# Kernel tuning notes

Measured on AMD Instinct MI355X. Metric: run time of the kernel, lower is better.

## Reference

```python
import jax, jax.numpy as jnp
from jax import lax
import numpy as np

LEVELS = 17
VAR_N = 4
UNITS = 3 * LEVELS          # 51 neurons: motor 17, command 13, inter 21
MOTOR = LEVELS
PRED_N = 4
UNFOLDS = 6                 # ncps LTC default ode_unfolds
EPS = 1e-8
B = 32768                   # recurrence length = B + PRED_N
D = VAR_N * LEVELS          # 68


def _build_wiring(seed=0):
    # AutoNCP(51, 17, sparsity_level=0.8): inter=21, command=13, motor=17
    # sensory_fanout=4, inter_fanout=2, 5 recurrent command synapses, motor_fanin=2
    rng = np.random.default_rng(seed)
    motor, command, S = 17, 13, LEVELS
    N = UNITS
    cmd = np.arange(motor, motor + command)
    intr = np.arange(motor + command, N)
    adj = np.zeros((N, N), np.float32)
    sadj = np.zeros((S, N), np.float32)
    pol = lambda: float(rng.choice([-1.0, 1.0]))
    for s in range(S):
        for d in rng.choice(intr, 4, replace=False):
            sadj[s, d] = pol()
    for d in intr:
        if not sadj[:, d].any():
            sadj[int(rng.integers(S)), d] = pol()
    for i in intr:
        for d in rng.choice(cmd, 2, replace=False):
            adj[i, d] = pol()
    for d in cmd:
        if not adj[intr, d].any():
            adj[int(rng.choice(intr)), d] = pol()
    for _ in range(5):
        adj[int(rng.choice(cmd)), int(rng.choice(cmd))] = pol()
    for m in range(motor):
        for srci in rng.choice(cmd, 2, replace=False):
            adj[srci, m] = pol()
    return adj, sadj


def setup_inputs():
    key = jax.random.key(0)
    ks = iter(jax.random.split(key, 48))
    u = lambda s, lo, hi: jax.random.uniform(next(ks), s, jnp.float32, lo, hi)
    lin = lambda i, o: jax.random.normal(next(ks), (i, o), jnp.float32) * (i ** -0.5)
    adj, sadj = _build_wiring()
    V, N, S = VAR_N, UNITS, LEVELS
    M1 = (LEVELS + D) // 2           # 42
    G = VAR_N * D                    # 272
    G2 = (G + D) // 2                # 170
    return dict(
        x=jax.random.normal(next(ks), (B, D), jnp.float32),
        pre_w1=lin(D, D), pre_b1=jnp.zeros((D,), jnp.float32),
        pre_w2=lin(D, D), pre_b2=jnp.zeros((D,), jnp.float32),
        gleak=u((V, N), 0.001, 1.0), vleak=u((V, N), -0.2, 0.2), cm=u((V, N), 0.4, 0.6),
        w=u((V, N, N), 0.001, 1.0), sigma=u((V, N, N), 3.0, 8.0), mu=u((V, N, N), 0.3, 0.8),
        erev=jnp.asarray(np.tile(adj, (V, 1, 1))),
        sens_w=u((V, S, N), 0.001, 1.0), sens_sigma=u((V, S, N), 3.0, 8.0), sens_mu=u((V, S, N), 0.3, 0.8),
        sens_erev=jnp.asarray(np.tile(sadj, (V, 1, 1))),
        in_w=jnp.ones((V, S), jnp.float32), in_b=jnp.zeros((V, S), jnp.float32),
        out_w=jnp.ones((V, MOTOR), jnp.float32), out_b=jnp.zeros((V, MOTOR), jnp.float32),
        tW1=lin(LEVELS, LEVELS), tb1=jnp.zeros((LEVELS,), jnp.float32),
        tW2=lin(LEVELS, M1), tb2=jnp.zeros((M1,), jnp.float32),
        tW3=lin(M1, D), tb3=jnp.zeros((D,), jnp.float32),
        gW1=lin(G, G), gb1=jnp.zeros((G,), jnp.float32),
        gW2=lin(G, G2), gb2=jnp.zeros((G2,), jnp.float32),
        gW3=lin(G2, D), gb3=jnp.zeros((D,), jnp.float32),
        mask=jnp.asarray((adj != 0).astype(np.float32)),
        sens_mask=jnp.asarray((sadj != 0).astype(np.float32)),
    )


def _forward(x, pre_w1, pre_b1, pre_w2, pre_b2,
             gleak, vleak, cm, w, sigma, mu, erev,
             sens_w, sens_sigma, sens_mu, sens_erev,
             in_w, in_b, out_w, out_b,
             tW1, tb1, tW2, tb2, tW3, tb3,
             gW1, gb1, gW2, gb2, gW3, gb3,
             mask, sens_mask, ckpt=False):
    sig = jax.nn.sigmoid
    # VarEncoder: Linear -> Sigmoid -> Linear
    h = sig(x @ pre_w1 + pre_b1) @ pre_w2 + pre_b2                  # (B, 68)
    xs = h.reshape(-1, VAR_N, LEVELS).transpose(1, 0, 2)            # (V, B, 17)
    seqs = jnp.concatenate([xs, jnp.repeat(xs[:, -1:, :], PRED_N, axis=1)], axis=1)  # (V, T, 17)

    def run(p, seq):
        gl_, vl_, cm_, w_, sg_, mu_, er_, sw_, ssg_, smu_, ser_, iw_, ib_, ow_, ob_ = p
        gl = jax.nn.softplus(gl_)                 # (N,)
        wp = jax.nn.softplus(w_) * mask           # (N, N) sparse NCP wiring
        swp = jax.nn.softplus(sw_) * sens_mask    # (S, N)
        cmt = jax.nn.softplus(cm_) * UNFOLDS      # cm / (elapsed=1 / unfolds)

        def step(v, u_in):
            u = u_in * iw_ + ib_                                   # affine input mapping
            sact = swp * sig((u[:, None] - smu_) * ssg_)           # (S, N)
            num_s = (sact * ser_).sum(0)
            den_s = sact.sum(0)

            def unfold(vv, _):
                wa = wp * sig((vv[:, None] - mu_) * sg_)           # (N, N), src axis 0
                vv = (cmt * vv + gl * vl_ + (wa * er_).sum(0) + num_s) / (
                    cmt + gl + wa.sum(0) + den_s + EPS)
                return vv, None

            v, _ = lax.scan(unfold, v, None, length=UNFOLDS)
            return v, v[:MOTOR] * ow_ + ob_                        # affine output mapping

        stepf = jax.checkpoint(step) if ckpt else step
        _, outs = lax.scan(stepf, jnp.zeros((UNITS,), seq.dtype), seq)
        return outs                                                # (T, 17)

    p = (gleak, vleak, cm, w, sigma, mu, erev,
         sens_w, sens_sigma, sens_mu, sens_erev, in_w, in_b, out_w, out_b)
    rs = jax.vmap(run, in_axes=(0, 0))(p, seqs)                    # (V, T, 17)
    r = rs.transpose(1, 0, 2)                                      # (T, V, 17)
    # CrossConnector: per-tile MLP 17->17->42->68 (sigmoids), flatten, 272->272->170->68
    t = sig(sig(sig(r @ tW1 + tb1) @ tW2 + tb2) @ tW3 + tb3)        # (T, V, 68)
    g = t.reshape(t.shape[0], -1)                                   # (T, 272)
    return sig(sig(g @ gW1 + gb1) @ gW2 + gb2) @ gW3 + gb3          # (T, 68)


def reference(x, pre_w1, pre_b1, pre_w2, pre_b2,
              gleak, vleak, cm, w, sigma, mu, erev,
              sens_w, sens_sigma, sens_mu, sens_erev,
              in_w, in_b, out_w, out_b,
              tW1, tb1, tW2, tb2, tW3, tb3,
              gW1, gb1, gW2, gb2, gW3, gb3,
              mask, sens_mask):
    return _forward(x, pre_w1, pre_b1, pre_w2, pre_b2,
                    gleak, vleak, cm, w, sigma, mu, erev,
                    sens_w, sens_sigma, sens_mu, sens_erev,
                    in_w, in_b, out_w, out_b,
                    tW1, tb1, tW2, tb2, tW3, tb3,
                    gW1, gb1, gW2, gb2, gW3, gb3,
                    mask, sens_mask)
```

## Files before the change

### kernel.cpp

```cpp
#include <hip/hip_runtime.h>
#include <hip/hip_bf16.h>
#include <math.h>

#define LEVELS 17
#define VARN   4
#define UNITS  51
#define MOTOR  17
#define NB     32768
#define TT     (NB + 4)
#define DD     68
#define LOG2E  1.4426950408889634f
#define TROWS  16

#define W_WARM  10
#define L_CHUNK 34
#define NCHUNK  ((TT + L_CHUNK - 1) / L_CHUNK)

#define W_F     64
#define L_F     64
#define NCHUNK_F ((TT + L_F - 1) / L_F)
#define CAP_R  16

#define MROWS  48
#define MBLK   ((TT + MROWS - 1) / MROWS)
#define EBLK   ((NB + MROWS - 1) / MROWS)
#define BUFSZ  (48 * 272 + 64)
#define EBUFSZ (48 * 72 + 64)

#define OFF_WA 0
#define OFF_WB 7680
#define OFF_WC 24576
#define OFF_WD 76800
#define OFF_WE 155136
#define OFF_WF 205824
#define OFF_P1 221184
#define OFF_P2 228864
#define WTS_SHORTS 236544
#define PSENS_N (VARN * LEVELS * UNITS)

typedef __attribute__((ext_vector_type(8))) short short8v;
typedef __attribute__((ext_vector_type(4))) float f32x4;

__device__ __forceinline__ float fast_rcp(float x) { return __builtin_amdgcn_rcpf(x); }
__device__ __forceinline__ float fast_exp2(float x) { return __builtin_amdgcn_exp2f(x); }
__device__ __forceinline__ float sigf(float x) { return fast_rcp(1.0f + __expf(-x)); }
__device__ __forceinline__ float softplusf(float x) { return logf(1.0f + expf(x)); }
__device__ __forceinline__ unsigned short f2bf(float x) {
    unsigned int u = __float_as_uint(x);
    unsigned int r = u + 0x7FFFu + ((u >> 16) & 1u);
    return (unsigned short)(r >> 16);
}

__global__ __launch_bounds__(256) void prep_weights(
    const float* __restrict__ tW1, const float* __restrict__ tW2, const float* __restrict__ tW3,
    const float* __restrict__ gW1, const float* __restrict__ gW2, const float* __restrict__ gW3,
    const float* __restrict__ pW1, const float* __restrict__ pW2,
    unsigned short* __restrict__ wts)
{
    const int ph = blockIdx.y;
    const int KTt[8]   = {3, 3, 6, 9, 9, 6, 3, 3};
    const int NCt[8]   = {5, 11, 17, 17, 11, 5, 5, 5};
    const int offsT[8] = {OFF_WA, OFF_WB, OFF_WC, OFF_WD, OFF_WE, OFF_WF, OFF_P1, OFF_P2};
    int S = NCt[ph] * KTt[ph] * 512;
    int idx = blockIdx.x * 256 + threadIdx.x;
    if (idx >= S) return;
    int tile = idx >> 9;
    int r    = idx & 511;
    int lane = r >> 3;
    int e    = r & 7;
    int KTp  = KTt[ph];
    int ct   = tile / KTp;
    int kt   = tile - ct * KTp;
    int n = ct * 16 + (lane & 15);
    int k = kt * 32 + (lane >> 4) * 8 + e;
    float val = 0.0f;
    switch (ph) {
        case 0: if (k < 68 && n < 68) { int v = k / 17; if (n / 17 == v) val = tW1[(k % 17) * 17 + (n % 17)]; } break;
        case 1: if (k < 68 && n < 168) { int v = k / 17; int c = n - 42 * v; if (c >= 0 && c < 42) val = tW2[(k % 17) * 42 + c]; } break;
        case 2: if (k < 168 && n < 272) { int v = k / 42; int c = n - 68 * v; if (c >= 0 && c < 68) val = tW3[(k % 42) * 68 + c]; } break;
        case 3: if (k < 272 && n < 272) val = gW1[k * 272 + n]; break;
        case 4: if (k < 272 && n < 170) val = gW2[k * 170 + n]; break;
        case 5: if (k < 170 && n < 68)  val = gW3[k * 68 + n]; break;
        case 6: if (k < 68 && n < 68)   val = pW1[k * 68 + n]; break;
        case 7: if (k < 68 && n < 68)   val = pW2[k * 68 + n]; break;
    }
    wts[offsT[ph] + idx] = f2bf(val);
}

__global__ __launch_bounds__(256) void prep_sens(
    const float* __restrict__ sens_w, const float* __restrict__ sens_sigma,
    const float* __restrict__ sens_mu, const float* __restrict__ sens_erev,
    float4* __restrict__ psens)
{
    int idx = blockIdx.x * 256 + threadIdx.x;
    if (idx >= PSENS_N) return;
    float sg = sens_sigma[idx], m = sens_mu[idx];
    float wf = softplusf(sens_w[idx]);
    psens[idx] = make_float4(fast_exp2(sg * m * LOG2E), -sg * LOG2E, wf, wf * sens_erev[idx]);
}

template<int KT, int NC>
__device__ __forceinline__ void mfma_phase(
    const unsigned short* __restrict__ wt,
    const unsigned short* __restrict__ bufIn, int ldkIn,
    unsigned short* __restrict__ bufOut, int ldkOut,
    const float* __restrict__ bias, int bmod, int Nvalid,
    int lane, int wave)
{
    #pragma unroll
    for (int rt = 0; rt < 3; ++rt) {
        short8v af[KT];
        int abase = (rt * 16 + (lane & 15)) * ldkIn + 8 * (lane >> 4);
        #pragma unroll
        for (int kt = 0; kt < KT; ++kt)
            af[kt] = *reinterpret_cast<const short8v*>(&bufIn[abase + kt * 32]);
        for (int ct = wave; ct < NC; ct += 4) {
            int c = ct * 16 + (lane & 15);
            const unsigned short* wp = wt + (size_t)(ct * KT) * 512 + lane * 8;
            short8v bf[KT];
            #pragma unroll
            for (int kt = 0; kt < KT; ++kt)
                bf[kt] = *reinterpret_cast<const short8v*>(&wp[kt * 512]);
            f32x4 acc = {0.0f, 0.0f, 0.0f, 0.0f};
            #pragma unroll
            for (int kt = 0; kt < KT; ++kt)
                acc = __builtin_amdgcn_mfma_f32_16x16x32_bf16(af[kt], bf[kt], acc, 0, 0, 0);
            float bv = 0.0f;
            if (c < Nvalid) {
                int cb = (bmod == 0) ? (c % 17) : (bmod == 1) ? (c % 42) : (bmod == 2) ? (c % 68) : c;
                bv = bias[cb];
            }
            #pragma unroll
            for (int i = 0; i < 4; ++i) {
                float vv = sigf(acc[i] + bv);
                int rl = rt * 16 + (lane >> 4) * 4 + i;
                if (c < ldkOut) bufOut[rl * ldkOut + c] = f2bf(vv);
            }
        }
    }
}

template<int KT>
__device__ __forceinline__ void mfma_final(
    const unsigned short* __restrict__ wt,
    const unsigned short* __restrict__ bufIn, int ldkIn,
    float* __restrict__ io, int baseRow,
    const float* __restrict__ gb3, int lane, int wave)
{
    #pragma unroll
    for (int rt = 0; rt < 3; ++rt) {
        short8v af[KT];
        int abase = (rt * 16 + (lane & 15)) * ldkIn + 8 * (lane >> 4);
        #pragma unroll
        for (int kt = 0; kt < KT; ++kt)
            af[kt] = *reinterpret_cast<const short8v*>(&bufIn[abase + kt * 32]);
        for (int ct = wave; ct < 5; ct += 4) {
            int c = ct * 16 + (lane & 15);
            const unsigned short* wp = wt + (size_t)(ct * KT) * 512 + lane * 8;
            short8v bf[KT];
            #pragma unroll
            for (int kt = 0; kt < KT; ++kt)
                bf[kt] = *reinterpret_cast<const short8v*>(&wp[kt * 512]);
            f32x4 acc = {0.0f, 0.0f, 0.0f, 0.0f};
            #pragma unroll
            for (int kt = 0; kt < KT; ++kt)
                acc = __builtin_amdgcn_mfma_f32_16x16x32_bf16(af[kt], bf[kt], acc, 0, 0, 0);
            float bv = (c < 68) ? gb3[c] : 0.0f;
            #pragma unroll
            for (int i = 0; i < 4; ++i) {
                int row = baseRow + rt * 16 + (lane >> 4) * 4 + i;
                if (c < 68 && row < TT) io[(size_t)row * DD + c] = acc[i] + bv;
            }
        }
    }
}

__global__ __launch_bounds__(256) void mlp_mfma(
    float* __restrict__ io, const unsigned short* __restrict__ wts,
    const float* __restrict__ tb1, const float* __restrict__ tb2, const float* __restrict__ tb3,
    const float* __restrict__ gb1, const float* __restrict__ gb2, const float* __restrict__ gb3)
{
    __shared__ unsigned short buf0[BUFSZ];
    __shared__ unsigned short buf1[BUFSZ];
    int tid = threadIdx.x, lane = tid & 63, wave = tid >> 6;
    int baseRow = blockIdx.x * MROWS;

    for (int e = tid; e < BUFSZ; e += 256) { buf0[e] = 0; buf1[e] = 0; }
    __syncthreads();
    for (int e = tid; e < MROWS * DD; e += 256) {
        int r = e / DD, c = e % DD;
        int gr = baseRow + r;
        float xv = (gr < TT) ? io[(size_t)gr * DD + c] : 0.0f;
        buf0[r * 72 + c] = f2bf(xv);
    }
    __syncthreads();
    mfma_phase<3, 5 >(wts + OFF_WA, buf0, 72,  buf1, 72,  tb1, 0, 68,  lane, wave); __syncthreads();
    mfma_phase<3, 11>(wts + OFF_WB, buf1, 72,  buf0, 168, tb2, 1, 168, lane, wave); __syncthreads();
    mfma_phase<6, 17>(wts + OFF_WC, buf0, 168, buf1, 272, tb3, 2, 272, lane, wave); __syncthreads();
    mfma_phase<9, 17>(wts + OFF_WD, buf1, 272, buf0, 272, gb1, 3, 272, lane, wave); __syncthreads();
    mfma_phase<9, 11>(wts + OFF_WE, buf0, 272, buf1, 176, gb2, 3, 170, lane, wave); __syncthreads();
    mfma_final<6>(wts + OFF_WF, buf1, 176, io, baseRow, gb3, lane, wave);
}

__global__ __launch_bounds__(256) void enc_mfma(
    const float* __restrict__ x, const unsigned short* __restrict__ wts,
    const float* __restrict__ pb1, const float* __restrict__ pb2,
    float* __restrict__ seq)
{
    __shared__ unsigned short buf0[EBUFSZ];
    __shared__ unsigned short buf1[EBUFSZ];
    int tid = threadIdx.x, lane = tid & 63, wave = tid >> 6;
    int baseRow = blockIdx.x * MROWS;

    for (int e = tid; e < EBUFSZ; e += 256) { buf0[e] = 0; buf1[e] = 0; }
    __syncthreads();
    for (int e = tid; e < MROWS * DD; e += 256) {
        int r = e / DD, c = e % DD;
        int gr = baseRow + r;
        float xv = (gr < NB) ? x[(size_t)gr * DD + c] : 0.0f;
        buf0[r * 72 + c] = f2bf(xv);
    }
    __syncthreads();
    mfma_phase<3, 5>(wts + OFF_P1, buf0, 72, buf1, 72, pb1, 3, 68, lane, wave);
    __syncthreads();
    #pragma unroll
    for (int rt = 0; rt < 3; ++rt) {
        short8v af[3];
        int abase = (rt * 16 + (lane & 15)) * 72 + 8 * (lane >> 4);
        #pragma unroll
        for (int kt = 0; kt < 3; ++kt)
            af[kt] = *reinterpret_cast<const short8v*>(&buf1[abase + kt * 32]);
        for (int ct = wave; ct < 5; ct += 4) {
            int c = ct * 16 + (lane & 15);
            const unsigned short* wp = wts + OFF_P2 + (size_t)(ct * 3) * 512 + lane * 8;
            short8v bf[3];
            #pragma unroll
            for (int kt = 0; kt < 3; ++kt)
                bf[kt] = *reinterpret_cast<const short8v*>(&wp[kt * 512]);
            f32x4 acc = {0.0f, 0.0f, 0.0f, 0.0f};
            #pragma unroll
            for (int kt = 0; kt < 3; ++kt)
                acc = __builtin_amdgcn_mfma_f32_16x16x32_bf16(af[kt], bf[kt], acc, 0, 0, 0);
            float bv = (c < 68) ? pb2[c] : 0.0f;
            #pragma unroll
            for (int i = 0; i < 4; ++i) {
                int row = baseRow + rt * 16 + (lane >> 4) * 4 + i;
                if (c < 68 && row < NB) {
                    float vv = acc[i] + bv;
                    int v = c / 17, s = c % 17;
                    float* dst = seq + ((size_t)v * TT + row) * LEVELS + s;
                    dst[0] = vv;
                    if (row == NB - 1) {
                        dst[1 * LEVELS] = vv; dst[2 * LEVELS] = vv;
                        dst[3 * LEVELS] = vv; dst[4 * LEVELS] = vv;
                    }
                }
            }
        }
    }
}

#define SENS_TPW 16
__global__ __launch_bounds__(256) void sens_kernel(
    const float* __restrict__ seq,
    const float4* __restrict__ psens,
    const float* __restrict__ in_w, const float* __restrict__ in_b,
    const float* __restrict__ sens_mask,
    float2* __restrict__ tab)
{
    int gwi = blockIdx.x * 4 + (threadIdx.x >> 6);
    int j   = threadIdx.x & 63;
    int v    = gwi & 3;
    int tbase = (gwi >> 2) * SENS_TPW;
    if (tbase >= TT) return;

    unsigned int bits0 = 0;
    if (j < UNITS)
        for (int s = 0; s < LEVELS; ++s)
            bits0 |= (sens_mask[s * UNITS + j] != 0.0f ? 1u : 0u) << s;
    int ns = __popc(bits0);
    int mS = ns;
    #pragma unroll
    for (int off = 32; off; off >>= 1) mS = max(mS, __shfl_xor(mS, off, 64));

    float iw = (j < LEVELS) ? in_w[v * LEVELS + j] : 0.0f;
    float ib = (j < LEVELS) ? in_b[v * LEVELS + j] : 0.0f;

    int tend = min(TT, tbase + SENS_TPW);
    for (int t = tbase; t < tend; ++t) {
        float u = (j < LEVELS)
            ? fmaf(seq[((size_t)v * TT + t) * LEVELS + j], iw, ib) : 0.0f;
        unsigned int bits = bits0;
        float num = 0.0f, den = 0.0f;
        for (int k = 0; k < mS; ++k) {
            bool on = (k < ns) && (bits != 0u);
            int s = on ? (__ffs(bits) - 1) : 0;
            if (on) bits &= bits - 1;
            float us = __shfl(u, s, 64);
            float4 p = psens[(v * LEVELS + s) * UNITS + (j < UNITS ? j : 0)];
            float g = fast_rcp(fmaf(p.x, fast_exp2(p.y * us), 1.0f));
            if (on) { num = fmaf(p.w, g, num); den = fmaf(p.z, g, den); }
        }
        if (j < UNITS)
            tab[((size_t)v * TT + t) * UNITS + j] = make_float2(num, den);
    }
}

template<int MH>
__device__ void scan_body(
    int j, int jn, bool hasHelp, int partner, int myStart, int myCnt,
    unsigned long long colbits, int v, int t0, int wstart, int tend,
    float cmt, float glvl, float cgl, float ow, float ob, bool isHelper,
    const float* __restrict__ w, const float* __restrict__ sigma,
    const float* __restrict__ mu, const float* __restrict__ erev,
    const float2* __restrict__ tab, float* __restrict__ rout)
{
    int   src[MH]; float fw[MH], fc[MH], fk[MH], fwfe[MH];
    unsigned long long bits = colbits;
    for (int s = 0; s < myStart; ++s) bits &= bits - 1;
    #pragma unroll
    for (int k = 0; k < MH; ++k) {
        bool on = (k < myCnt);
        int sc = on ? (__ffsll((unsigned long long)bits) - 1) : 0;
        src[k] = sc;
        size_t pi = ((size_t)v * UNITS + sc) * UNITS + jn;
        float sg = on ? sigma[pi] : 0.0f;
        float m  = on ? mu[pi]    : 0.0f;
        fw[k] = on ? softplusf(w[pi]) : 0.0f;
        fc[k] = fast_exp2(sg * m * LOG2E);
        fk[k] = -sg * LOG2E;
        fwfe[k] = on ? fw[k] * erev[pi] : 0.0f;
        if (on) bits &= bits - 1;
    }
    const float2* tp = tab + (size_t)v * TT * UNITS + jn;
    float* rp = rout + (size_t)v * LEVELS + j;
    float2 nd = tp[(size_t)t0 * UNITS];
    float vreg = 0.0f;
    for (int t = t0; t < tend; ++t) {
        float2 ndc = nd;
        if (t + 1 < tend) nd = tp[(size_t)(t + 1) * UNITS];
        float bn = isHelper ? 0.0f : (glvl + ndc.x);
        float bd = isHelper ? 0.0f : (cgl + ndc.y);
        #pragma unroll
        for (int uf = 0; uf < 6; ++uf) {
            float vs[MH];
            #pragma unroll
            for (int k = 0; k < MH; ++k) vs[k] = __shfl(vreg, src[k], 64);
            float num = bn, den = bd;
            #pragma unroll
            for (int k = 0; k < MH; ++k) {
                float g = fast_rcp(fmaf(fc[k], fast_exp2(fk[k] * vs[k]), 1.0f));
                num = fmaf(fwfe[k], g, num);
                den = fmaf(fw[k], g, den);
            }
            float pn = __shfl(num, partner, 64);
            float pd = __shfl(den, partner, 64);
            if (hasHelp) { num += pn; den += pd; }
            vreg = fmaf(cmt, vreg, num) * fast_rcp(den);
        }
        if (j < MOTOR && t >= wstart) rp[(size_t)t * DD] = fmaf(vreg, ow, ob);
    }
}

__device__ void scan_body_gen(
    int j, int jn, bool hasHelp, int partner, int myStart, int myCnt, int mcMax,
    unsigned long long colbits, int v, int t0, int wstart, int tend,
    float cmt, float glvl, float cgl, float ow, float ob, bool isHelper,
    const float* __restrict__ w, const float* __restrict__ sigma,
    const float* __restrict__ mu, const float* __restrict__ erev,
    const float2* __restrict__ tab, float* __restrict__ rout)
{
    unsigned long long mybits = colbits;
    for (int s = 0; s < myStart; ++s) mybits &= mybits - 1;
    const float2* tp = tab + (size_t)v * TT * UNITS + jn;
    float* rp = rout + (size_t)v * LEVELS + j;
    float vreg = 0.0f;
    for (int t = t0; t < tend; ++t) {
        float2 ndc = tp[(size_t)t * UNITS];
        float bn = isHelper ? 0.0f : (glvl + ndc.x);
        float bd = isHelper ? 0.0f : (cgl + ndc.y);
        for (int uf = 0; uf < 6; ++uf) {
            unsigned long long bits = mybits;
            float num = bn, den = bd;
            for (int k = 0; k < mcMax; ++k) {
                bool on = (k < myCnt) && (bits != 0ull);
                int sc = on ? (__ffsll(bits) - 1) : 0;
                if (on) bits &= bits - 1;
                float vs = __shfl(vreg, sc, 64);
                size_t pi = ((size_t)v * UNITS + sc) * UNITS + jn;
                float a = on ? softplusf(w[pi]) * sigf((vs - mu[pi]) * sigma[pi]) : 0.0f;
                num = fmaf(a, on ? erev[pi] : 0.0f, num);
                den += a;
            }
            float pn = __shfl(num, partner, 64);
            float pd = __shfl(den, partner, 64);
            if (hasHelp) { num += pn; den += pd; }
            vreg = fmaf(cmt, vreg, num) * fast_rcp(den);
        }
        if (j < MOTOR && t >= wstart) rp[(size_t)t * DD] = fmaf(vreg, ow, ob);
    }
}

__global__ __launch_bounds__(256, 8) void scan_pre(
    const float2* __restrict__ tab,
    const float* __restrict__ gleak, const float* __restrict__ vleak, const float* __restrict__ cm,
    const float* __restrict__ w, const float* __restrict__ sigma,
    const float* __restrict__ mu, const float* __restrict__ erev,
    const float* __restrict__ out_w, const float* __restrict__ out_b,
    const float* __restrict__ mask,
    float* __restrict__ rout)
{
    int gwi = (blockIdx.x << 2) + (threadIdx.x >> 6);
    int j = threadIdx.x & 63;
    int v = gwi & 3;
    int chunk = gwi >> 2;
    if (chunk >= NCHUNK) return;
    int wstart = chunk * L_CHUNK;
    int tend = min(TT, wstart + L_CHUNK);
    int t0 = max(0, wstart - W_WARM);

    bool isHelper = (j >= UNITS);
    int jn = isHelper ? (j - 34) : j;
    unsigned long long colbits = 0ull;
    for (int i = 0; i < UNITS; ++i)
        colbits |= (unsigned long long)(mask[i * UNITS + jn] != 0.0f ? 1 : 0) << i;
    int nf = __popcll(colbits);
    bool isCmd = (jn >= MOTOR && jn < MOTOR + 13);
    int nh = (nf + 1) >> 1;
    int myStart, myCnt;
    if (isHelper)    { myStart = nh; myCnt = nf - nh; }
    else if (isCmd)  { myStart = 0;  myCnt = nh; }
    else             { myStart = 0;  myCnt = nf; }
    bool hasHelp = (!isHelper) && isCmd;
    int partner = hasHelp ? (jn + 34) : j;

    float cmt  = softplusf(cm[v * UNITS + jn]) * 6.0f;
    float gl   = softplusf(gleak[v * UNITS + jn]);
    float glvl = gl * vleak[v * UNITS + jn];
    float cgl  = cmt + gl + 1e-8f;
    float ow = (j < MOTOR) ? out_w[v * LEVELS + j] : 0.0f;
    float ob = (j < MOTOR) ? out_b[v * LEVELS + j] : 0.0f;

    int mc = myCnt;
    #pragma unroll
    for (int off = 32; off; off >>= 1) mc = max(mc, __shfl_xor(mc, off, 64));

    if (mc <= 4)
        scan_body<4>(j, jn, hasHelp, partner, myStart, myCnt, colbits, v, t0, wstart, tend,
                     cmt, glvl, cgl, ow, ob, isHelper, w, sigma, mu, erev, tab, rout);
    else if (mc <= 6)
        scan_body<6>(j, jn, hasHelp, partner, myStart, myCnt, colbits, v, t0, wstart, tend,
                     cmt, glvl, cgl, ow, ob, isHelper, w, sigma, mu, erev, tab, rout);
    else if (mc <= 8)
        scan_body<8>(j, jn, hasHelp, partner, myStart, myCnt, colbits, v, t0, wstart, tend,
                     cmt, glvl, cgl, ow, ob, isHelper, w, sigma, mu, erev, tab, rout);
    else
        scan_body_gen(j, jn, hasHelp, partner, myStart, myCnt, mc, colbits, v, t0, wstart, tend,
                      cmt, glvl, cgl, ow, ob, isHelper, w, sigma, mu, erev, tab, rout);
}

__global__ __launch_bounds__(128) void enc_kernel(
    const float* __restrict__ x,
    const float* __restrict__ W1, const float* __restrict__ b1,
    const float* __restrict__ W2, const float* __restrict__ b2,
    float* __restrict__ seq)
{
    int t = blockIdx.x;
    int j = threadIdx.x;
    __shared__ float xs[DD];
    __shared__ float h1[DD];
    if (j < DD) xs[j] = x[(size_t)t * DD + j];
    __syncthreads();
    if (j < DD) {
        float acc = b1[j];
        #pragma unroll 4
        for (int k = 0; k < DD; ++k) acc = fmaf(xs[k], W1[k * DD + j], acc);
        h1[j] = sigf(acc);
    }
    __syncthreads();
    if (j < DD) {
        float acc = b2[j];
        #pragma unroll 4
        for (int k = 0; k < DD; ++k) acc = fmaf(h1[k], W2[k * DD + j], acc);
        int v = j / LEVELS, s = j % LEVELS;
        float* dst = seq + ((size_t)v * TT + t) * LEVELS + s;
        dst[0] = acc;
        if (t == NB - 1) {
            dst[1 * LEVELS] = acc; dst[2 * LEVELS] = acc;
            dst[3 * LEVELS] = acc; dst[4 * LEVELS] = acc;
        }
    }
}

template<int MF, int MS>
__device__ __forceinline__ void scan_loop_f(
    int j, int v, int t0, int wstart, int tend,
    const float* __restrict__ seq, float* __restrict__ rout,
    float cmt, float glvl, float cgl, float iw, float ib, float ow, float ob,
    int nf, int ns,
    const int* rs_, const float* rw_, const float* rc_, const float* rk_, const float* re_,
    const int* ss_, const float* sw_, const float* sc_, const float* sk_, const float* se_)
{
    int fs[MF]; float fw[MF], fc[MF], fk[MF], fe[MF];
    #pragma unroll
    for (int k = 0; k < MF; ++k) {
        bool on = k < nf;
        int idx = j * CAP_R + k;
        fs[k] = on ? rs_[idx] : 0;
        fw[k] = on ? rw_[idx] : 0.0f;
        fc[k] = on ? rc_[idx] : 1.0f;
        fk[k] = on ? rk_[idx] : 0.0f;
        fe[k] = on ? re_[idx] : 0.0f;
    }
    int gs[MS]; float gw[MS], gc[MS], gk[MS], ge[MS];
    #pragma unroll
    for (int k = 0; k < MS; ++k) {
        bool on = k < ns;
        int idx = j * LEVELS + k;
        gs[k] = on ? ss_[idx] : 0;
        gw[k] = on ? sw_[idx] : 0.0f;
        gc[k] = on ? sc_[idx] : 1.0f;
        gk[k] = on ? sk_[idx] : 0.0f;
        ge[k] = on ? se_[idx] : 0.0f;
    }
    const float* sp = seq + (size_t)v * TT * LEVELS + j;
    float* rp = rout + (size_t)v * LEVELS + j;
    float xnext = (j < LEVELS) ? sp[(size_t)t0 * LEVELS] : 0.0f;
    float vreg = 0.0f;
    for (int t = t0; t < tend; ++t) {
        float u = fmaf(xnext, iw, ib);
        if (j < LEVELS && t + 1 < tend) xnext = sp[(size_t)(t + 1) * LEVELS];
        float us[MS];
        #pragma unroll
        for (int k = 0; k < MS; ++k) us[k] = __shfl(u, gs[k], 64);
        float sa[MS];
        #pragma unroll
        for (int k = 0; k < MS; ++k)
            sa[k] = gw[k] * fast_rcp(fmaf(gc[k], fast_exp2(gk[k] * us[k]), 1.0f));
        float bn = glvl, bd = cgl;
        #pragma unroll
        for (int k = 0; k < MS; ++k) { bn = fmaf(sa[k], ge[k], bn); bd += sa[k]; }
        #pragma unroll
        for (int uf = 0; uf < 6; ++uf) {
            float vsa[MF];
            #pragma unroll
            for (int k = 0; k < MF; ++k) vsa[k] = __shfl(vreg, fs[k], 64);
            float aa[MF];
            #pragma unroll
            for (int k = 0; k < MF; ++k)
                aa[k] = fw[k] * fast_rcp(fmaf(fc[k], fast_exp2(fk[k] * vsa[k]), 1.0f));
            float num = bn, den = bd;
            #pragma unroll
            for (int k = 0; k < MF; ++k) { num = fmaf(aa[k], fe[k], num); den += aa[k]; }
            vreg = fmaf(cmt, vreg, num) * fast_rcp(den);
        }
        if (j < LEVELS && t >= wstart) rp[(size_t)t * DD] = fmaf(vreg, ow, ob);
    }
}

__global__ __launch_bounds__(64) void scan_fallback(
    const float* __restrict__ seq,
    const float* __restrict__ gleak, const float* __restrict__ vleak, const float* __restrict__ cm,
    const float* __restrict__ w, const float* __restrict__ sigma,
    const float* __restrict__ mu, const float* __restrict__ erev,
    const float* __restrict__ sens_w, const float* __restrict__ sens_sigma,
    const float* __restrict__ sens_mu, const float* __restrict__ sens_erev,
    const float* __restrict__ in_w, const float* __restrict__ in_b,
    const float* __restrict__ out_w, const float* __restrict__ out_b,
    const float* __restrict__ mask, const float* __restrict__ sens_mask,
    float* __restrict__ rout)
{
    __shared__ int   rs_[UNITS * CAP_R];
    __shared__ float rw_[UNITS * CAP_R], rc_[UNITS * CAP_R], rk_[UNITS * CAP_R], re_[UNITS * CAP_R];
    __shared__ int   ss_[UNITS * LEVELS];
    __shared__ float sw_[UNITS * LEVELS], sc_[UNITS * LEVELS], sk_[UNITS * LEVELS], se_[UNITS * LEVELS];
    __shared__ int   cnts[64], scnts[64];
    __shared__ int   red[2];

    int j = threadIdx.x;
    int v = blockIdx.x & 3;
    int chunk = blockIdx.x >> 2;
    int wstart = chunk * L_F;
    if (wstart >= TT) return;
    int tend = min(TT, wstart + L_F);
    int t0 = max(0, wstart - W_F);

    int nf = 0, ns = 0;
    if (j < UNITS) {
        for (int i = 0; i < UNITS; ++i) {
            if (mask[i * UNITS + j] != 0.0f) {
                if (nf < CAP_R) {
                    size_t pi = ((size_t)v * UNITS + i) * UNITS + j;
                    int idx = j * CAP_R + nf;
                    float sg = sigma[pi], m = mu[pi];
                    rs_[idx] = i;
                    rw_[idx] = softplusf(w[pi]);
                    rc_[idx] = fast_exp2(sg * m * LOG2E);
                    rk_[idx] = -sg * LOG2E;
                    re_[idx] = erev[pi];
                }
                nf++;
            }
        }
        for (int s = 0; s < LEVELS; ++s) {
            if (sens_mask[s * UNITS + j] != 0.0f) {
                size_t pi = ((size_t)v * LEVELS + s) * UNITS + j;
                int idx = j * LEVELS + ns;
                float sg = sens_sigma[pi], m = sens_mu[pi];
                ss_[idx] = s;
                sw_[idx] = softplusf(sens_w[pi]);
                sc_[idx] = fast_exp2(sg * m * LOG2E);
                sk_[idx] = -sg * LOG2E;
                se_[idx] = sens_erev[pi];
                ns++;
            }
        }
    }
    cnts[j] = nf; scnts[j] = ns;
    __syncthreads();
    if (j == 0) {
        int mf = 0, ms = 0;
        for (int i = 0; i < UNITS; ++i) { mf = max(mf, cnts[i]); ms = max(ms, scnts[i]); }
        red[0] = mf; red[1] = ms;
    }
    __syncthreads();
    int maxF = red[0], maxS = red[1];

    int jc = (j < UNITS) ? j : (UNITS - 1);
    float cmt  = softplusf(cm[v * UNITS + jc]) * 6.0f;
    float gl   = softplusf(gleak[v * UNITS + jc]);
    float glvl = gl * vleak[v * UNITS + jc];
    float cgl  = cmt + gl + 1e-8f;
    float iw = (j < LEVELS) ? in_w[v * LEVELS + j]  : 0.0f;
    float ib = (j < LEVELS) ? in_b[v * LEVELS + j]  : 0.0f;
    float ow = (j < LEVELS) ? out_w[v * LEVELS + j] : 0.0f;
    float ob = (j < LEVELS) ? out_b[v * LEVELS + j] : 0.0f;

    if (maxF <= 11 && maxS <= 12)
        scan_loop_f<11, 12>(j, v, t0, wstart, tend, seq, rout, cmt, glvl, cgl, iw, ib, ow, ob, nf, ns,
                            rs_, rw_, rc_, rk_, re_, ss_, sw_, sc_, sk_, se_);
    else
        scan_loop_f<16, 17>(j, v, t0, wstart, tend, seq, rout, cmt, glvl, cgl, iw, ib, ow, ob, nf, ns,
                            rs_, rw_, rc_, rk_, re_, ss_, sw_, sc_, sk_, se_);
}

__global__ __launch_bounds__(256) void mlp_kernel(
    float* __restrict__ io,
    const float* __restrict__ tW1, const float* __restrict__ tb1,
    const float* __restrict__ tW2, const float* __restrict__ tb2,
    const float* __restrict__ tW3, const float* __restrict__ tb3,
    const float* __restrict__ gW1, const float* __restrict__ gb1,
    const float* __restrict__ gW2, const float* __restrict__ gb2,
    const float* __restrict__ gW3, const float* __restrict__ gb3)
{
    __shared__ __align__(16) float A[TROWS][272];
    __shared__ __align__(16) float Bf[TROWS][272];
    int base = blockIdx.x * TROWS;
    int tid = threadIdx.x;

    for (int e = tid; e < TROWS * DD; e += 256) {
        int r = e / DD, c = e % DD;
        A[r][c] = (base + r < TT) ? io[(size_t)(base + r) * DD + c] : 0.0f;
    }
    __syncthreads();
    for (int c = tid; c < 4 * LEVELS; c += 256) {
        int vv = c / LEVELS, cc = c % LEVELS;
        float acc[TROWS]; float bias = tb1[cc];
        #pragma unroll
        for (int r = 0; r < TROWS; ++r) acc[r] = bias;
        for (int k = 0; k < LEVELS; ++k) {
            float wv = tW1[k * LEVELS + cc];
            #pragma unroll
            for (int r = 0; r < TROWS; ++r) acc[r] = fmaf(A[r][vv * LEVELS + k], wv, acc[r]);
        }
        #pragma unroll
        for (int r = 0; r < TROWS; ++r) Bf[r][c] = sigf(acc[r]);
    }
    __syncthreads();
    for (int c = tid; c < 4 * 42; c += 256) {
        int vv = c / 42, cc = c % 42;
        float acc[TROWS]; float bias = tb2[cc];
        #pragma unroll
        for (int r = 0; r < TROWS; ++r) acc[r] = bias;
        for (int k = 0; k < LEVELS; ++k) {
            float wv = tW2[k * 42 + cc];
            #pragma unroll
            for (int r = 0; r < TROWS; ++r) acc[r] = fmaf(Bf[r][vv * LEVELS + k], wv, acc[r]);
        }
        #pragma unroll
        for (int r = 0; r < TROWS; ++r) A[r][vv * 42 + cc] = sigf(acc[r]);
    }
    __syncthreads();
    for (int c = tid; c < 4 * DD; c += 256) {
        int vv = c / DD, cc = c % DD;
        float acc[TROWS]; float bias = tb3[cc];
        #pragma unroll
        for (int r = 0; r < TROWS; ++r) acc[r] = bias;
        for (int k = 0; k < 42; ++k) {
            float wv = tW3[k * DD + cc];
            #pragma unroll
            for (int r = 0; r < TROWS; ++r) acc[r] = fmaf(A[r][vv * 42 + k], wv, acc[r]);
        }
        #pragma unroll
        for (int r = 0; r < TROWS; ++r) Bf[r][c] = sigf(acc[r]);
    }
    __syncthreads();
    for (int c = tid; c < 272; c += 256) {
        float acc[TROWS]; float bias = gb1[c];
        #pragma unroll
        for (int r = 0; r < TROWS; ++r) acc[r] = bias;
        for (int k = 0; k < 272; k += 4) {
            float w0 = gW1[(k + 0) * 272 + c];
            float w1 = gW1[(k + 1) * 272 + c];
            float w2 = gW1[(k + 2) * 272 + c];
            float w3 = gW1[(k + 3) * 272 + c];
            #pragma unroll
            for (int r = 0; r < TROWS; ++r) {
                float4 g4 = *reinterpret_cast<const float4*>(&Bf[r][k]);
                acc[r] = fmaf(g4.x, w0, fmaf(g4.y, w1, fmaf(g4.z, w2, fmaf(g4.w, w3, acc[r]))));
            }
        }
        #pragma unroll
        for (int r = 0; r < TROWS; ++r) A[r][c] = sigf(acc[r]);
    }
    __syncthreads();
    for (int c = tid; c < 170; c += 256) {
        float acc[TROWS]; float bias = gb2[c];
        #pragma unroll
        for (int r = 0; r < TROWS; ++r) acc[r] = bias;
        for (int k = 0; k < 272; k += 4) {
            float w0 = gW2[(k + 0) * 170 + c];
            float w1 = gW2[(k + 1) * 170 + c];
            float w2 = gW2[(k + 2) * 170 + c];
            float w3 = gW2[(k + 3) * 170 + c];
            #pragma unroll
            for (int r = 0; r < TROWS; ++r) {
                float4 g4 = *reinterpret_cast<const float4*>(&A[r][k]);
                acc[r] = fmaf(g4.x, w0, fmaf(g4.y, w1, fmaf(g4.z, w2, fmaf(g4.w, w3, acc[r]))));
            }
        }
        #pragma unroll
        for (int r = 0; r < TROWS; ++r) Bf[r][c] = sigf(acc[r]);
    }
    __syncthreads();
    for (int c = tid; c < DD; c += 256) {
        float acc[TROWS]; float bias = gb3[c];
        #pragma unroll
        for (int r = 0; r < TROWS; ++r) acc[r] = bias;
        for (int k = 0; k < 168; k += 4) {
            float w0 = gW3[(k + 0) * DD + c];
            float w1 = gW3[(k + 1) * DD + c];
            float w2 = gW3[(k + 2) * DD + c];
            float w3 = gW3[(k + 3) * DD + c];
            #pragma unroll
            for (int r = 0; r < TROWS; ++r) {
                float4 g4 = *reinterpret_cast<const float4*>(&Bf[r][k]);
                acc[r] = fmaf(g4.x, w0, fmaf(g4.y, w1, fmaf(g4.z, w2, fmaf(g4.w, w3, acc[r]))));
            }
        }
        for (int k = 168; k < 170; ++k) {
            float wv = gW3[k * DD + c];
            #pragma unroll
            for (int r = 0; r < TROWS; ++r) acc[r] = fmaf(Bf[r][k], wv, acc[r]);
        }
        #pragma unroll
        for (int r = 0; r < TROWS; ++r)
            if (base + r < TT) io[(size_t)(base + r) * DD + c] = acc[r];
    }
}

extern "C" void kernel_launch(void* const* d_in, const int* in_sizes, int n_in,
                              void* d_out, int out_size, void* d_ws, size_t ws_size,
                              hipStream_t stream)
{
    (void)in_sizes; (void)n_in; (void)out_size;
    const float* x        = (const float*)d_in[0];
    const float* pre_w1   = (const float*)d_in[1];
    const float* pre_b1   = (const float*)d_in[2];
    const float* pre_w2   = (const float*)d_in[3];
    const float* pre_b2   = (const float*)d_in[4];
    const float* gleak    = (const float*)d_in[5];
    const float* vleak    = (const float*)d_in[6];
    const float* cm       = (const float*)d_in[7];
    const float* w        = (const float*)d_in[8];
    const float* sigma    = (const float*)d_in[9];
    const float* mu       = (const float*)d_in[10];
    const float* erev     = (const float*)d_in[11];
    const float* sens_w   = (const float*)d_in[12];
    const float* sens_sig = (const float*)d_in[13];
    const float* sens_mu  = (const float*)d_in[14];
    const float* sens_er  = (const float*)d_in[15];
    const float* in_w     = (const float*)d_in[16];
    const float* in_b     = (const float*)d_in[17];
    const float* out_w    = (const float*)d_in[18];
    const float* out_b    = (const float*)d_in[19];
    const float* tW1      = (const float*)d_in[20];
    const float* tb1      = (const float*)d_in[21];
    const float* tW2      = (const float*)d_in[22];
    const float* tb2      = (const float*)d_in[23];
    const float* tW3      = (const float*)d_in[24];
    const float* tb3      = (const float*)d_in[25];
    const float* gW1      = (const float*)d_in[26];
    const float* gb1      = (const float*)d_in[27];
    const float* gW2      = (const float*)d_in[28];
    const float* gb2      = (const float*)d_in[29];
    const float* gW3      = (const float*)d_in[30];
    const float* gb3      = (const float*)d_in[31];
    const float* mask     = (const float*)d_in[32];
    const float* smask    = (const float*)d_in[33];

    float* out = (float*)d_out;

    size_t tab_bytes = (size_t)VARN * TT * UNITS * sizeof(float2);
    size_t seq_bytes = (size_t)VARN * TT * LEVELS * sizeof(float);
    size_t wts_bytes = (size_t)WTS_SHORTS * sizeof(unsigned short);
    size_t ps_bytes  = (size_t)PSENS_N * sizeof(float4);

    if (ws_size >= tab_bytes + seq_bytes + wts_bytes + ps_bytes) {
        float2* tab = (float2*)d_ws;
        float*  seq = (float*)((char*)d_ws + tab_bytes);
        unsigned short* wts = (unsigned short*)((char*)d_ws + tab_bytes + seq_bytes);
        float4* psens = (float4*)((char*)d_ws + tab_bytes + seq_bytes + wts_bytes);
        prep_weights<<<dim3(306, 8), 256, 0, stream>>>(
            tW1, tW2, tW3, gW1, gW2, gW3, pre_w1, pre_w2, wts);
        prep_sens<<<(PSENS_N + 255) / 256, 256, 0, stream>>>(
            sens_w, sens_sig, sens_mu, sens_er, psens);
        enc_mfma<<<EBLK, 256, 0, stream>>>(x, wts, pre_b1, pre_b2, seq);
        {
            int slabs = (TT + SENS_TPW - 1) / SENS_TPW;
            int waves = slabs * VARN;
            sens_kernel<<<(waves + 3) / 4, 256, 0, stream>>>(
                seq, psens, in_w, in_b, smask, tab);
        }
        scan_pre<<<NCHUNK, 256, 0, stream>>>(
            tab, gleak, vleak, cm, w, sigma, mu, erev, out_w, out_b, mask, out);
        mlp_mfma<<<MBLK, 256, 0, stream>>>(out, wts, tb1, tb2, tb3, gb1, gb2, gb3);
    } else if (ws_size >= seq_bytes) {
        float* seq = (float*)d_ws;
        enc_kernel<<<NB, 128, 0, stream>>>(x, pre_w1, pre_b1, pre_w2, pre_b2, seq);
        scan_fallback<<<VARN * NCHUNK_F, 64, 0, stream>>>(
            seq, gleak, vleak, cm, w, sigma, mu, erev,
            sens_w, sens_sig, sens_mu, sens_er,
            in_w, in_b, out_w, out_b, mask, smask, out);
        mlp_kernel<<<(TT + TROWS - 1) / TROWS, 256, 0, stream>>>(
            out, tW1, tb1, tW2, tb2, tW3, tb3, gW1, gb1, gW2, gb2, gW3, gb3);
    }
}
```

Measured before the change: 251.4 us.

## Split command-neuron synapse sums across three lanes in LTC scan

```diff
diff --git a/kernel.cpp b/kernel.cpp
--- a/kernel.cpp
+++ b/kernel.cpp
@@ -307,10 +307,11 @@
 }
 
 template<int MH>
-__device__ void scan_body(
-    int j, int jn, bool hasHelp, int partner, int myStart, int myCnt,
+__device__ void scan_body3(
+    int j, int jnS, int jnV, float ownMul, float helpMul, int h1, int h2,
+    int myStart, int myCnt, bool isH1,
     unsigned long long colbits, int v, int t0, int wstart, int tend,
-    float cmt, float glvl, float cgl, float ow, float ob, bool isHelper,
+    float cmt, float glvl, float cgl, float ow, float ob,
     const float* __restrict__ w, const float* __restrict__ sigma,
     const float* __restrict__ mu, const float* __restrict__ erev,
     const float2* __restrict__ tab, float* __restrict__ rout)
@@ -323,7 +324,7 @@
         bool on = (k < myCnt);
         int sc = on ? (__ffsll((unsigned long long)bits) - 1) : 0;
         src[k] = sc;
-        size_t pi = ((size_t)v * UNITS + sc) * UNITS + jn;
+        size_t pi = ((size_t)v * UNITS + sc) * UNITS + jnS;
         float sg = on ? sigma[pi] : 0.0f;
         float m  = on ? mu[pi]    : 0.0f;
         fw[k] = on ? softplusf(w[pi]) : 0.0f;
@@ -332,30 +333,33 @@
         fwfe[k] = on ? fw[k] * erev[pi] : 0.0f;
         if (on) bits &= bits - 1;
     }
-    const float2* tp = tab + (size_t)v * TT * UNITS + jn;
+    const float2* tp = tab + (size_t)v * TT * UNITS + jnV;
     float* rp = rout + (size_t)v * LEVELS + j;
     float2 nd = tp[(size_t)t0 * UNITS];
     float vreg = 0.0f;
     for (int t = t0; t < tend; ++t) {
         float2 ndc = nd;
         if (t + 1 < tend) nd = tp[(size_t)(t + 1) * UNITS];
-        float bn = isHelper ? 0.0f : (glvl + ndc.x);
-        float bd = isHelper ? 0.0f : (cgl + ndc.y);
+        float bn = isH1 ? 0.0f : (glvl + ndc.x);
+        float bd = isH1 ? 1.0f : (cgl + ndc.y);
         #pragma unroll
         for (int uf = 0; uf < 6; ++uf) {
             float vs[MH];
             #pragma unroll
             for (int k = 0; k < MH; ++k) vs[k] = __shfl(vreg, src[k], 64);
-            float num = bn, den = bd;
+            float accn = 0.0f, accd = 0.0f;
             #pragma unroll
             for (int k = 0; k < MH; ++k) {
                 float g = fast_rcp(fmaf(fc[k], fast_exp2(fk[k] * vs[k]), 1.0f));
-                num = fmaf(fwfe[k], g, num);
-                den = fmaf(fw[k], g, den);
-            }
-            float pn = __shfl(num, partner, 64);
-            float pd = __shfl(den, partner, 64);
-            if (hasHelp) { num += pn; den += pd; }
+                accn = fmaf(fwfe[k], g, accn);
+                accd = fmaf(fw[k], g, accd);
+            }
+            float p1n = __shfl(accn, h1, 64);
+            float p1d = __shfl(accd, h1, 64);
+            float p2n = __shfl(accn, h2, 64);
+            float p2d = __shfl(accd, h2, 64);
+            float num = fmaf(accn, ownMul, bn) + helpMul * (p1n + p2n);
+            float den = fmaf(accd, ownMul, bd) + helpMul * (p1d + p2d);
             vreg = fmaf(cmt, vreg, num) * fast_rcp(den);
         }
         if (j < MOTOR && t >= wstart) rp[(size_t)t * DD] = fmaf(vreg, ow, ob);
@@ -419,24 +423,42 @@
     int tend = min(TT, wstart + L_CHUNK);
     int t0 = max(0, wstart - W_WARM);
 
-    bool isHelper = (j >= UNITS);
-    int jn = isHelper ? (j - 34) : j;
+    bool isH1   = (j >= UNITS);
+    bool isH2   = (j >= 30 && j < 43);
+    bool isCmdL = (j >= MOTOR && j < 30);
+    int jnV = isH1 ? (j - 34) : j;
+    int jnS = isH1 ? (j - 34) : (isH2 ? (j - 13) : j);
+
     unsigned long long colbits = 0ull;
     for (int i = 0; i < UNITS; ++i)
-        colbits |= (unsigned long long)(mask[i * UNITS + jn] != 0.0f ? 1 : 0) << i;
+        colbits |= (unsigned long long)(mask[i * UNITS + jnS] != 0.0f ? 1 : 0) << i;
     int nf = __popcll(colbits);
-    bool isCmd = (jn >= MOTOR && jn < MOTOR + 13);
-    int nh = (nf + 1) >> 1;
+
+    int ownIn = 0;
+    if (j >= 30 && j < UNITS) {
+        for (int i = 0; i < UNITS; ++i)
+            ownIn |= (mask[i * UNITS + j] != 0.0f ? 1 : 0);
+    }
+    int bad = ownIn;
+    #pragma unroll
+    for (int off = 32; off; off >>= 1) bad |= __shfl_xor(bad, off, 64);
+
+    int n1 = (nf + 2) / 3;
+    int n2 = (nf - n1 + 1) / 2;
+    int n3 = nf - n1 - n2;
     int myStart, myCnt;
-    if (isHelper)    { myStart = nh; myCnt = nf - nh; }
-    else if (isCmd)  { myStart = 0;  myCnt = nh; }
-    else             { myStart = 0;  myCnt = nf; }
-    bool hasHelp = (!isHelper) && isCmd;
-    int partner = hasHelp ? (jn + 34) : j;
-
-    float cmt  = softplusf(cm[v * UNITS + jn]) * 6.0f;
-    float gl   = softplusf(gleak[v * UNITS + jn]);
-    float glvl = gl * vleak[v * UNITS + jn];
+    if (isH1)        { myStart = n1 + n2; myCnt = n3; }
+    else if (isH2)   { myStart = n1;      myCnt = n2; }
+    else if (isCmdL) { myStart = 0;       myCnt = n1; }
+    else             { myStart = 0;       myCnt = nf; }
+    float ownMul  = (isH1 || isH2) ? 0.0f : 1.0f;
+    float helpMul = isCmdL ? 1.0f : 0.0f;
+    int h1 = isCmdL ? (j + 34) : j;
+    int h2 = isCmdL ? (j + 13) : j;
+
+    float cmt  = softplusf(cm[v * UNITS + jnV]) * 6.0f;
+    float gl   = softplusf(gleak[v * UNITS + jnV]);
+    float glvl = gl * vleak[v * UNITS + jnV];
     float cgl  = cmt + gl + 1e-8f;
     float ow = (j < MOTOR) ? out_w[v * LEVELS + j] : 0.0f;
     float ob = (j < MOTOR) ? out_b[v * LEVELS + j] : 0.0f;
@@ -445,18 +467,42 @@
     #pragma unroll
     for (int off = 32; off; off >>= 1) mc = max(mc, __shfl_xor(mc, off, 64));
 
-    if (mc <= 4)
-        scan_body<4>(j, jn, hasHelp, partner, myStart, myCnt, colbits, v, t0, wstart, tend,
-                     cmt, glvl, cgl, ow, ob, isHelper, w, sigma, mu, erev, tab, rout);
-    else if (mc <= 6)
-        scan_body<6>(j, jn, hasHelp, partner, myStart, myCnt, colbits, v, t0, wstart, tend,
-                     cmt, glvl, cgl, ow, ob, isHelper, w, sigma, mu, erev, tab, rout);
-    else if (mc <= 8)
-        scan_body<8>(j, jn, hasHelp, partner, myStart, myCnt, colbits, v, t0, wstart, tend,
-                     cmt, glvl, cgl, ow, ob, isHelper, w, sigma, mu, erev, tab, rout);
-    else
-        scan_body_gen(j, jn, hasHelp, partner, myStart, myCnt, mc, colbits, v, t0, wstart, tend,
-                      cmt, glvl, cgl, ow, ob, isHelper, w, sigma, mu, erev, tab, rout);
+    if (!bad && mc <= 2)
+        scan_body3<2>(j, jnS, jnV, ownMul, helpMul, h1, h2, myStart, myCnt, isH1,
+                      colbits, v, t0, wstart, tend, cmt, glvl, cgl, ow, ob,
+                      w, sigma, mu, erev, tab, rout);
+    else if (!bad && mc <= 3)
+        scan_body3<3>(j, jnS, jnV, ownMul, helpMul, h1, h2, myStart, myCnt, isH1,
+                      colbits, v, t0, wstart, tend, cmt, glvl, cgl, ow, ob,
+                      w, sigma, mu, erev, tab, rout);
+    else if (!bad && mc <= 4)
+        scan_body3<4>(j, jnS, jnV, ownMul, helpMul, h1, h2, myStart, myCnt, isH1,
+                      colbits, v, t0, wstart, tend, cmt, glvl, cgl, ow, ob,
+                      w, sigma, mu, erev, tab, rout);
+    else {
+        int jn = isH1 ? (j - 34) : j;
+        unsigned long long cb = 0ull;
+        for (int i = 0; i < UNITS; ++i)
+            cb |= (unsigned long long)(mask[i * UNITS + jn] != 0.0f ? 1 : 0) << i;
+        int nfg = __popcll(cb);
+        bool isCmd = (jn >= MOTOR && jn < 30);
+        int nh = (nfg + 1) >> 1;
+        int gs, gc;
+        if (isH1)      { gs = nh; gc = nfg - nh; }
+        else if (isCmd){ gs = 0;  gc = nh; }
+        else           { gs = 0;  gc = nfg; }
+        bool hasHelp = (!isH1) && isCmd;
+        int partner = hasHelp ? (jn + 34) : j;
+        float cmtg  = softplusf(cm[v * UNITS + jn]) * 6.0f;
+        float glg   = softplusf(gleak[v * UNITS + jn]);
+        float glvlg = glg * vleak[v * UNITS + jn];
+        float cglg  = cmtg + glg + 1e-8f;
+        int mg = gc;
+        #pragma unroll
+        for (int off = 32; off; off >>= 1) mg = max(mg, __shfl_xor(mg, off, 64));
+        scan_body_gen(j, jn, hasHelp, partner, gs, gc, mg, cb, v, t0, wstart, tend,
+                      cmtg, glvlg, cglg, ow, ob, isH1, w, sigma, mu, erev, tab, rout);
+    }
 }
 
 __global__ __launch_bounds__(128) void enc_kernel(
```

After: 225.7 us. 1.11x faster.
